# Kernel tuning notes

Measured on AMD Instinct MI355X. Metric: run time of the kernel, lower is better.

The kernel has to match this reference:

```python
import jax, jax.numpy as jnp
import numpy as np

B, S, H, NH = 2, 2048, 2048, 16
HD = H // NH

def setup_inputs() -> dict:
    key = jax.random.key(0)
    ks = jax.random.split(key, 6)
    scale = 1.0 / np.sqrt(H)
    return {
        "x": jax.random.normal(ks[0], (B, S, H), dtype=jnp.float32),
        "Wq": jax.random.normal(ks[1], (H, H), dtype=jnp.float32) * scale,
        "Wk": jax.random.normal(ks[2], (H, H), dtype=jnp.float32) * scale,
        "Wv": jax.random.normal(ks[3], (H, H), dtype=jnp.float32) * scale,
        "Wo": jax.random.normal(ks[4], (H, H), dtype=jnp.float32) * scale,
        "bo": jax.random.normal(ks[5], (H,), dtype=jnp.float32) * 0.01,
    }

def reference(x, Wq, Wk, Wv, Wo, bo):
    # nn.Linear convention: y = x @ W.T (W is [out, in])
    q = (x @ Wq.T).reshape(B, S, NH, HD).transpose(0, 2, 1, 3)  # [B,NH,S,HD]
    k = (x @ Wk.T).reshape(B, S, NH, HD).transpose(0, 2, 1, 3)
    v = (x @ Wv.T).reshape(B, S, NH, HD).transpose(0, 2, 1, 3)
    scale = jnp.asarray(HD, x.dtype) ** -0.5
    scores = jnp.einsum('bhqd,bhkd->bhqk', q, k) * scale  # [B,NH,S,S]
    attn = jax.nn.softmax(scores, axis=-1)
    out = jnp.einsum('bhqk,bhkd->bhqd', attn, v)  # [B,NH,S,HD]
    out = out.transpose(0, 2, 1, 3).reshape(B, S, H)
    return out @ Wo.T + bo
```

## Files before the change

kernel.cpp:

```cpp
#include <hip/hip_runtime.h>
#include <hip/hip_bf16.h>
#include <stdint.h>

#define S_LEN 2048
#define NHEADS 16
#define HDIM 128
#define H_TOT 2048
#define BATCH 2
#define M_TOK 4096
#define KDIM 2048

typedef __attribute__((ext_vector_type(8))) short bf16x8;
typedef __attribute__((ext_vector_type(4))) float f32x4;
typedef __attribute__((ext_vector_type(16))) float f32x16;

__device__ inline ushort bf16rn(float f) {
  union { float f; uint32_t u; } x; x.f = f;
  uint32_t r = x.u + 0x7FFF + ((x.u >> 16) & 1);
  return (ushort)(r >> 16);
}

__global__ __launch_bounds__(256) void cvt_bf16_kernel(const float* __restrict__ in,
                                                       ushort* __restrict__ out, int n4) {
  int i = blockIdx.x * blockDim.x + threadIdx.x;
  int stride = gridDim.x * blockDim.x;
  for (; i < n4; i += stride) {
    float4 v = reinterpret_cast<const float4*>(in)[i];
    ushort4 o;
    o.x = bf16rn(v.x); o.y = bf16rn(v.y); o.z = bf16rn(v.z); o.w = bf16rn(v.w);
    reinterpret_cast<ushort4*>(out)[i] = o;
  }
}

__global__ __launch_bounds__(256) void cvt4_bf16_kernel(const float* __restrict__ w0,
                                                        const float* __restrict__ w1,
                                                        const float* __restrict__ w2,
                                                        const float* __restrict__ w3,
                                                        ushort* __restrict__ o0,
                                                        ushort* __restrict__ o1,
                                                        ushort* __restrict__ o2,
                                                        ushort* __restrict__ o3) {
  const int N4 = KDIM * KDIM / 4;
  int i = blockIdx.x * blockDim.x + threadIdx.x;
  int stride = gridDim.x * blockDim.x;
  for (; i < 4 * N4; i += stride) {
    int seg = i >> 20, off = i & (N4 - 1);
    const float* in = (seg == 0) ? w0 : (seg == 1) ? w1 : (seg == 2) ? w2 : w3;
    ushort* out = (seg == 0) ? o0 : (seg == 1) ? o1 : (seg == 2) ? o2 : o3;
    float4 v = reinterpret_cast<const float4*>(in)[off];
    ushort4 o;
    o.x = bf16rn(v.x); o.y = bf16rn(v.y); o.z = bf16rn(v.z); o.w = bf16rn(v.w);
    reinterpret_cast<ushort4*>(out)[off] = o;
  }
}

template<int MODE>
__global__ __launch_bounds__(256) void gemm_nt(const ushort* __restrict__ A,
                                               const ushort* __restrict__ Bw,
                                               void* __restrict__ Cout,
                                               const float* __restrict__ bias,
                                               float scale) {
  __shared__ ushort As[128 * 32];
  __shared__ ushort Bs[128 * 32];
  const int K = KDIM;
  int tid = threadIdx.x;
  int wave = tid >> 6, lane = tid & 63;
  int bid = blockIdx.x;
  int c = bid & 7, ii = bid >> 3;
  int bx = (c & 1) * 8 + (ii & 7);
  int by = (c >> 1) * 8 + (ii >> 3);
  int bm = by * 128, bn = bx * 128;
  int wr = wave >> 1, wc = wave & 1;

  f32x4 acc[4][4];
#pragma unroll
  for (int i = 0; i < 4; i++)
#pragma unroll
    for (int j = 0; j < 4; j++) acc[i][j] = (f32x4){0.f, 0.f, 0.f, 0.f};

  int r0 = wave * 32 + (lane >> 2);
  int c8 = (lane & 3) * 8;
  const ushort* gA0 = A + (size_t)(bm + r0) * K + c8;
  const ushort* gA1 = gA0 + 16 * (size_t)K;
  const ushort* gB0 = Bw + (size_t)(bn + r0) * K + c8;
  const ushort* gB1 = gB0 + 16 * (size_t)K;
  ushort* lA0 = As + (wave * 2 + 0) * 512;
  ushort* lA1 = As + (wave * 2 + 1) * 512;
  ushort* lB0 = Bs + (wave * 2 + 0) * 512;
  ushort* lB1 = Bs + (wave * 2 + 1) * 512;

  int aoff = (wr * 64 + (lane & 15)) * 32 + (lane >> 4) * 8;
  int boff = (wc * 64 + (lane & 15)) * 32 + (lane >> 4) * 8;

  for (int kt = 0; kt < K; kt += 32) {
    __builtin_amdgcn_global_load_lds((const __attribute__((address_space(1))) void*)gA0,
                                     (__attribute__((address_space(3))) void*)lA0, 16, 0, 0);
    __builtin_amdgcn_global_load_lds((const __attribute__((address_space(1))) void*)gA1,
                                     (__attribute__((address_space(3))) void*)lA1, 16, 0, 0);
    __builtin_amdgcn_global_load_lds((const __attribute__((address_space(1))) void*)gB0,
                                     (__attribute__((address_space(3))) void*)lB0, 16, 0, 0);
    __builtin_amdgcn_global_load_lds((const __attribute__((address_space(1))) void*)gB1,
                                     (__attribute__((address_space(3))) void*)lB1, 16, 0, 0);
    __syncthreads();

    bf16x8 af[4], bfm[4];
#pragma unroll
    for (int i = 0; i < 4; i++) af[i] = *reinterpret_cast<const bf16x8*>(&As[aoff + i * 512]);
#pragma unroll
    for (int j = 0; j < 4; j++) bfm[j] = *reinterpret_cast<const bf16x8*>(&Bs[boff + j * 512]);
#pragma unroll
    for (int i = 0; i < 4; i++)
#pragma unroll
      for (int j = 0; j < 4; j++)
        acc[i][j] = __builtin_amdgcn_mfma_f32_16x16x32_bf16(af[i], bfm[j], acc[i][j], 0, 0, 0);
    __syncthreads();

    gA0 += 32; gA1 += 32; gB0 += 32; gB1 += 32;
  }

  int rbase = bm + wr * 64 + (lane >> 4) * 4;
  int cbase = bn + wc * 64 + (lane & 15);
  if (MODE == 2) {
    float* Cf = (float*)Cout;
#pragma unroll
    for (int j = 0; j < 4; j++) {
      int n = cbase + j * 16;
      float bv = bias[n];
#pragma unroll
      for (int i = 0; i < 4; i++)
#pragma unroll
        for (int q = 0; q < 4; q++) {
          int m = rbase + i * 16 + q;
          Cf[(size_t)m * H_TOT + n] = acc[i][j][q] + bv;
        }
    }
  } else {
    ushort* Cb = (ushort*)Cout;
#pragma unroll
    for (int j = 0; j < 4; j++) {
      int n = cbase + j * 16;
      int h = n >> 7, d = n & 127;
#pragma unroll
      for (int i = 0; i < 4; i++)
#pragma unroll
        for (int q = 0; q < 4; q++) {
          int m = rbase + i * 16 + q;
          int b = m >> 11, s = m & 2047;
          int bh = b * NHEADS + h;
          size_t idx;
          if (MODE == 0) {
            idx = (((size_t)(bh * 64 + (s >> 5)) * 8 + (d >> 4)) * 64 +
                   ((d >> 3) & 1) * 32 + (s & 31)) * 8 + (d & 7);
          } else {
            int r = s & 15;
            int e = (r & 3) | ((r >> 1) & 4);
            int hi = (r >> 2) & 1;
            idx = (((size_t)(bh * 64 + (s >> 5)) * 8 + ((s >> 4) & 1) * 4 + (d >> 5)) * 64 +
                   hi * 32 + (d & 31)) * 8 + e;
          }
          Cb[idx] = bf16rn(acc[i][j][q] * scale);
        }
    }
  }
}

__global__ __launch_bounds__(128) void attn_kernel(const ushort* __restrict__ Qf,
                                                   const ushort* __restrict__ Kf,
                                                   const ushort* __restrict__ Vf,
                                                   ushort* __restrict__ Ob) {
  __shared__ __attribute__((aligned(16))) ushort KV[2][8192];
  __shared__ float lsinv[2][32];
  int lane = threadIdx.x & 63, wave = threadIdx.x >> 6;
  int hi = lane >> 5;

  int bid = blockIdx.x;
  int swz = (bid & 7) * 128 + (bid >> 3);
  int bh = swz >> 5, qt = swz & 31;
  int b = bh >> 4, h = bh & 15;
  int qrow0 = qt * 64 + wave * 32;

  const bf16x8* Qv = reinterpret_cast<const bf16x8*>(Qf) +
                     ((size_t)(bh * 64 + qt * 2 + wave) * 8) * 64 + lane;
  bf16x8 qf[8];
#pragma unroll
  for (int kc = 0; kc < 8; kc++) qf[kc] = Qv[kc * 64];

  f32x16 oacc[4];
#pragma unroll
  for (int d32 = 0; d32 < 4; d32++)
#pragma unroll
    for (int r = 0; r < 16; r++) oacc[d32][r] = 0.f;
  float lsum = 0.f;
  int laneoff = lane * 8;
  const ushort* sbase = wave ? Vf : Kf;

#define STAGE(kt, bufsel)                                                                   \
  {                                                                                         \
    size_t gc = ((size_t)(bh * 64 + (kt))) * 8;                                             \
    _Pragma("unroll") for (int i_ = 0; i_ < 8; i_++) {                                      \
      __builtin_amdgcn_global_load_lds(                                                     \
          (const __attribute__((address_space(1))) void*)(sbase + (gc + i_) * 512 + laneoff),\
          (__attribute__((address_space(3))) void*)(&KV[bufsel][(wave * 8 + i_) * 512]),    \
          16, 0, 0);                                                                        \
    }                                                                                       \
  }

  union pu { bf16x8 v; uint32_t u[4]; };
  pu paA0, paA1, paB0, paB1;
  bf16x8 vrA[8], vrB[8];
  const bf16x8 bz = {0, 0, 0, 0, 0, 0, 0, 0};
#pragma unroll
  for (int j = 0; j < 4; j++) { paA0.u[j] = 0; paA1.u[j] = 0; }
#pragma unroll
  for (int i = 0; i < 8; i++) vrA[i] = bz;

  STAGE(0, 0);
  asm volatile("s_waitcnt vmcnt(0)" ::: "memory");
  __syncthreads();

  const int NT = S_LEN / 32;

#define BODY(T, PI0, PI1, VI, PO0, PO1, VO)                                                 \
  {                                                                                         \
    if ((T) + 1 < NT) STAGE((T) + 1, ((T) + 1) & 1);                                        \
    const ushort* lb = &KV[(T) & 1][0];                                                     \
    f32x16 S;                                                                               \
    _Pragma("unroll") for (int r = 0; r < 16; r++) S[r] = 0.f;                              \
    __builtin_amdgcn_s_setprio(1);                                                          \
    _Pragma("unroll") for (int kc = 0; kc < 8; kc++) {                                      \
      bf16x8 kfr = *reinterpret_cast<const bf16x8*>(&lb[kc * 512 + laneoff]);               \
      S = __builtin_amdgcn_mfma_f32_32x32x16_bf16(kfr, qf[kc], S, 0, 0, 0);                 \
    }                                                                                       \
    _Pragma("unroll") for (int d32 = 0; d32 < 4; d32++) {                                   \
      oacc[d32] = __builtin_amdgcn_mfma_f32_32x32x16_bf16(PI0.v, VI[d32], oacc[d32], 0, 0, 0); \
      oacc[d32] = __builtin_amdgcn_mfma_f32_32x32x16_bf16(PI1.v, VI[4 + d32], oacc[d32], 0, 0, 0); \
    }                                                                                       \
    __builtin_amdgcn_s_setprio(0);                                                          \
    float p_[16];                                                                           \
    _Pragma("unroll") for (int r = 0; r < 16; r++) { p_[r] = exp2f(S[r]); lsum += p_[r]; }  \
    _Pragma("unroll") for (int j = 0; j < 4; j++) {                                         \
      uint32_t w0_, w1_;                                                                    \
      asm("v_cvt_pk_bf16_f32 %0, %1, %2" : "=v"(w0_) : "v"(p_[2 * j]), "v"(p_[2 * j + 1])); \
      asm("v_cvt_pk_bf16_f32 %0, %1, %2" : "=v"(w1_) : "v"(p_[8 + 2 * j]), "v"(p_[9 + 2 * j])); \
      PO0.u[j] = w0_; PO1.u[j] = w1_;                                                       \
    }                                                                                       \
    _Pragma("unroll") for (int i_ = 0; i_ < 8; i_++)                                        \
      VO[i_] = *reinterpret_cast<const bf16x8*>(&lb[4096 + i_ * 512 + laneoff]);            \
    asm volatile("s_waitcnt vmcnt(0)" ::: "memory");                                        \
    __syncthreads();                                                                        \
  }

  for (int t = 0; t < NT; t += 2) {
    BODY(t,     paA0, paA1, vrA, paB0, paB1, vrB);
    BODY(t + 1, paB0, paB1, vrB, paA0, paA1, vrA);
  }
#pragma unroll
  for (int d32 = 0; d32 < 4; d32++) {
    oacc[d32] = __builtin_amdgcn_mfma_f32_32x32x16_bf16(paA0.v, vrA[d32], oacc[d32], 0, 0, 0);
    oacc[d32] = __builtin_amdgcn_mfma_f32_32x32x16_bf16(paA1.v, vrA[4 + d32], oacc[d32], 0, 0, 0);
  }

  float total = lsum + __shfl_xor(lsum, 32);
  if (lane < 32) lsinv[wave][lane] = 1.0f / total;
  __syncthreads();

  float ls[16];
#pragma unroll
  for (int r = 0; r < 16; r++) ls[r] = lsinv[wave][(r & 3) + 8 * (r >> 2) + 4 * hi];
#pragma unroll
  for (int d32 = 0; d32 < 4; d32++)
#pragma unroll
    for (int r = 0; r < 16; r++) {
      int row = (r & 3) + 8 * (r >> 2) + 4 * hi;
      size_t idx = ((size_t)(b * S_LEN + qrow0 + row)) * H_TOT + h * HDIM + d32 * 32 + (lane & 31);
      Ob[idx] = bf16rn(oacc[d32][r] * ls[r]);
    }
#undef BODY
#undef STAGE
}

extern "C" void kernel_launch(void* const* d_in, const int* in_sizes, int n_in,
                              void* d_out, int out_size, void* d_ws, size_t ws_size,
                              hipStream_t stream) {
  const float* x  = (const float*)d_in[0];
  const float* Wq = (const float*)d_in[1];
  const float* Wk = (const float*)d_in[2];
  const float* Wv = (const float*)d_in[3];
  const float* Wo = (const float*)d_in[4];
  const float* bo = (const float*)d_in[5];
  float* out = (float*)d_out;

  char* w = (char*)d_ws;
  ushort* xb  = (ushort*)w; w += (size_t)M_TOK * KDIM * 2;
  ushort* Wqb = (ushort*)w; w += (size_t)KDIM * KDIM * 2;
  ushort* Wkb = (ushort*)w; w += (size_t)KDIM * KDIM * 2;
  ushort* Wvb = (ushort*)w; w += (size_t)KDIM * KDIM * 2;
  ushort* Wob = (ushort*)w; w += (size_t)KDIM * KDIM * 2;
  ushort* Qh  = (ushort*)w; w += (size_t)M_TOK * KDIM * 2;
  ushort* Kh  = (ushort*)w; w += (size_t)M_TOK * KDIM * 2;
  ushort* Vt  = (ushort*)w; w += (size_t)M_TOK * KDIM * 2;
  ushort* Ob  = (ushort*)w; w += (size_t)M_TOK * KDIM * 2;

  hipLaunchKernelGGL(cvt_bf16_kernel, dim3(2048), dim3(256), 0, stream, x, xb, M_TOK * KDIM / 4);
  hipLaunchKernelGGL(cvt4_bf16_kernel, dim3(2048), dim3(256), 0, stream,
                     Wq, Wk, Wv, Wo, Wqb, Wkb, Wvb, Wob);

  const float sl = 0.08838834764831845f * 1.4426950408889634f;
  dim3 g(512), blk(256);
  hipLaunchKernelGGL((gemm_nt<0>), g, blk, 0, stream, xb, Wqb, (void*)Qh, (const float*)nullptr, sl);
  hipLaunchKernelGGL((gemm_nt<0>), g, blk, 0, stream, xb, Wkb, (void*)Kh, (const float*)nullptr, 1.0f);
  hipLaunchKernelGGL((gemm_nt<1>), g, blk, 0, stream, xb, Wvb, (void*)Vt, (const float*)nullptr, 1.0f);

  hipLaunchKernelGGL(attn_kernel, dim3(1024), dim3(128), 0, stream, Qh, Kh, Vt, Ob);

  hipLaunchKernelGGL((gemm_nt<2>), g, blk, 0, stream, Ob, Wob, (void*)out, bo, 1.0f);
}
```

Before: 301.7 us.

## Fuse QKV projections into one pipelined, swizzled 128x256 GEMM kernel

Replaces the single-buffered 128x128 GEMM with a 512-thread 128x256 tile kernel. It uses a K-step of 64, triple-buffered LDS fed by async global-to-LDS loads, an XOR-swizzled LDS layout and waitcnt-based prefetch overlap. The three Q/K/V projections become one launch over a concatenated 6144-wide weight, relying on the contiguous workspace layout, with per-segment output routing and scaling. The aim is to hide global load latency, cut LDS bank conflicts, reduce barrier overhead per FLOP and remove two launches. In exchange it uses about 147KB of LDS per block, which limits occupancy to one block per CU, and it issues redundant prefetches of the first tiles at the end of the loop.

```diff
diff --git a/kernel.cpp b/kernel.cpp
--- a/kernel.cpp
+++ b/kernel.cpp
@@ -54,23 +54,55 @@
   }
 }
 
-template<int MODE>
-__global__ __launch_bounds__(256) void gemm_nt(const ushort* __restrict__ A,
-                                               const ushort* __restrict__ Bw,
-                                               void* __restrict__ Cout,
-                                               const float* __restrict__ bias,
-                                               float scale) {
-  __shared__ ushort As[128 * 32];
-  __shared__ ushort Bs[128 * 32];
+template<int MODE, int NBX>
+__global__ __launch_bounds__(512) void gemm2(const ushort* __restrict__ A,
+                                             const ushort* __restrict__ Bw,
+                                             void* __restrict__ C0,
+                                             void* __restrict__ C1,
+                                             void* __restrict__ C2,
+                                             const float* __restrict__ bias,
+                                             float scale) {
+  __shared__ __attribute__((aligned(16))) char lds[3 * 49152];
   const int K = KDIM;
+  const int NKT = K / 64;
   int tid = threadIdx.x;
   int wave = tid >> 6, lane = tid & 63;
+  int lanelo = lane & 15, lanehi = lane >> 4;
+  int wr = wave >> 2, wc = wave & 3;
+
   int bid = blockIdx.x;
-  int c = bid & 7, ii = bid >> 3;
-  int bx = (c & 1) * 8 + (ii & 7);
-  int by = (c >> 1) * 8 + (ii >> 3);
-  int bm = by * 128, bn = bx * 128;
-  int wr = wave >> 1, wc = wave & 1;
+  const int CHX = NBX / 8;
+  int ii = bid >> 3;
+  int bx = (bid & 7) * CHX + (ii % CHX);
+  int by = ii / CHX;
+  int bm = by * 128, bn = bx * 256;
+
+  const ushort* srcA[2];
+  const ushort* srcB[4];
+#pragma unroll
+  for (int i = 0; i < 2; i++) {
+    int c = i * 512 + tid, row = c >> 3, slot = c & 7;
+    srcA[i] = A + (size_t)(bm + row) * K + ((slot ^ (row & 7)) * 8);
+  }
+#pragma unroll
+  for (int i = 0; i < 4; i++) {
+    int c = i * 512 + tid, row = c >> 3, slot = c & 7;
+    srcB[i] = Bw + (size_t)(bn + row) * K + ((slot ^ (row & 7)) * 8);
+  }
+
+#define STAGE(tile, buf)                                                                    \
+  {                                                                                         \
+    char* dA = lds + (buf) * 49152 + (size_t)tid * 16;                                      \
+    char* dB = lds + (buf) * 49152 + 16384 + (size_t)tid * 16;                              \
+    _Pragma("unroll") for (int i_ = 0; i_ < 2; i_++)                                        \
+      __builtin_amdgcn_global_load_lds(                                                     \
+          (const __attribute__((address_space(1))) void*)(srcA[i_] + (tile) * 64),          \
+          (__attribute__((address_space(3))) void*)(dA + i_ * 8192), 16, 0, 0);             \
+    _Pragma("unroll") for (int i_ = 0; i_ < 4; i_++)                                        \
+      __builtin_amdgcn_global_load_lds(                                                     \
+          (const __attribute__((address_space(1))) void*)(srcB[i_] + (tile) * 64),          \
+          (__attribute__((address_space(3))) void*)(dB + i_ * 8192), 16, 0, 0);             \
+  }
 
   f32x4 acc[4][4];
 #pragma unroll
@@ -78,77 +110,82 @@
 #pragma unroll
     for (int j = 0; j < 4; j++) acc[i][j] = (f32x4){0.f, 0.f, 0.f, 0.f};
 
-  int r0 = wave * 32 + (lane >> 2);
-  int c8 = (lane & 3) * 8;
-  const ushort* gA0 = A + (size_t)(bm + r0) * K + c8;
-  const ushort* gA1 = gA0 + 16 * (size_t)K;
-  const ushort* gB0 = Bw + (size_t)(bn + r0) * K + c8;
-  const ushort* gB1 = gB0 + 16 * (size_t)K;
-  ushort* lA0 = As + (wave * 2 + 0) * 512;
-  ushort* lA1 = As + (wave * 2 + 1) * 512;
-  ushort* lB0 = Bs + (wave * 2 + 0) * 512;
-  ushort* lB1 = Bs + (wave * 2 + 1) * 512;
-
-  int aoff = (wr * 64 + (lane & 15)) * 32 + (lane >> 4) * 8;
-  int boff = (wc * 64 + (lane & 15)) * 32 + (lane >> 4) * 8;
-
-  for (int kt = 0; kt < K; kt += 32) {
-    __builtin_amdgcn_global_load_lds((const __attribute__((address_space(1))) void*)gA0,
-                                     (__attribute__((address_space(3))) void*)lA0, 16, 0, 0);
-    __builtin_amdgcn_global_load_lds((const __attribute__((address_space(1))) void*)gA1,
-                                     (__attribute__((address_space(3))) void*)lA1, 16, 0, 0);
-    __builtin_amdgcn_global_load_lds((const __attribute__((address_space(1))) void*)gB0,
-                                     (__attribute__((address_space(3))) void*)lB0, 16, 0, 0);
-    __builtin_amdgcn_global_load_lds((const __attribute__((address_space(1))) void*)gB1,
-                                     (__attribute__((address_space(3))) void*)lB1, 16, 0, 0);
-    __syncthreads();
-
-    bf16x8 af[4], bfm[4];
-#pragma unroll
-    for (int i = 0; i < 4; i++) af[i] = *reinterpret_cast<const bf16x8*>(&As[aoff + i * 512]);
-#pragma unroll
-    for (int j = 0; j < 4; j++) bfm[j] = *reinterpret_cast<const bf16x8*>(&Bs[boff + j * 512]);
-#pragma unroll
-    for (int i = 0; i < 4; i++)
-#pragma unroll
-      for (int j = 0; j < 4; j++)
-        acc[i][j] = __builtin_amdgcn_mfma_f32_16x16x32_bf16(af[i], bfm[j], acc[i][j], 0, 0, 0);
-    __syncthreads();
-
-    gA0 += 32; gA1 += 32; gB0 += 32; gB1 += 32;
-  }
-
-  int rbase = bm + wr * 64 + (lane >> 4) * 4;
-  int cbase = bn + wc * 64 + (lane & 15);
+  STAGE(0, 0);
+  STAGE(1, 1);
+  asm volatile("s_waitcnt vmcnt(6)" ::: "memory");
+  __builtin_amdgcn_s_barrier();
+  __builtin_amdgcn_sched_barrier(0);
+
+  for (int t = 0; t < NKT; t++) {
+    STAGE((t + 2) & (NKT - 1), (t + 2) % 3);
+
+    const ushort* bufc = (const ushort*)(lds + (t % 3) * 49152);
+
+    bf16x8 bfr[4][2];
+#pragma unroll
+    for (int nf = 0; nf < 4; nf++)
+#pragma unroll
+      for (int kh = 0; kh < 2; kh++) {
+        int row = wc * 64 + nf * 16 + lanelo;
+        int slot = (kh * 4 + lanehi) ^ (row & 7);
+        bfr[nf][kh] = *reinterpret_cast<const bf16x8*>(&bufc[8192 + row * 64 + slot * 8]);
+      }
+
+    __builtin_amdgcn_s_setprio(1);
+#pragma unroll
+    for (int mf = 0; mf < 4; mf++) {
+      int row = wr * 64 + mf * 16 + lanelo;
+      bf16x8 af[2];
+#pragma unroll
+      for (int kh = 0; kh < 2; kh++) {
+        int slot = (kh * 4 + lanehi) ^ (row & 7);
+        af[kh] = *reinterpret_cast<const bf16x8*>(&bufc[row * 64 + slot * 8]);
+      }
+#pragma unroll
+      for (int nf = 0; nf < 4; nf++)
+#pragma unroll
+        for (int kh = 0; kh < 2; kh++)
+          acc[mf][nf] = __builtin_amdgcn_mfma_f32_16x16x32_bf16(af[kh], bfr[nf][kh],
+                                                                acc[mf][nf], 0, 0, 0);
+    }
+    __builtin_amdgcn_s_setprio(0);
+
+    asm volatile("s_waitcnt vmcnt(6)" ::: "memory");
+    __builtin_amdgcn_s_barrier();
+    __builtin_amdgcn_sched_barrier(0);
+  }
+
   if (MODE == 2) {
-    float* Cf = (float*)Cout;
-#pragma unroll
-    for (int j = 0; j < 4; j++) {
-      int n = cbase + j * 16;
+    float* Cf = (float*)C0;
+#pragma unroll
+    for (int nf = 0; nf < 4; nf++) {
+      int n = bn + wc * 64 + nf * 16 + lanelo;
       float bv = bias[n];
 #pragma unroll
-      for (int i = 0; i < 4; i++)
+      for (int mf = 0; mf < 4; mf++)
 #pragma unroll
         for (int q = 0; q < 4; q++) {
-          int m = rbase + i * 16 + q;
-          Cf[(size_t)m * H_TOT + n] = acc[i][j][q] + bv;
+          int m = bm + wr * 64 + mf * 16 + lanehi * 4 + q;
+          Cf[(size_t)m * H_TOT + n] = acc[mf][nf][q] + bv;
         }
     }
   } else {
-    ushort* Cb = (ushort*)Cout;
-#pragma unroll
-    for (int j = 0; j < 4; j++) {
-      int n = cbase + j * 16;
+    int seg = bn >> 11;
+    ushort* dst = (seg == 0) ? (ushort*)C0 : (seg == 1) ? (ushort*)C1 : (ushort*)C2;
+    float sc = (seg == 0) ? scale : 1.0f;
+#pragma unroll
+    for (int nf = 0; nf < 4; nf++) {
+      int n = (bn & 2047) + wc * 64 + nf * 16 + lanelo;
       int h = n >> 7, d = n & 127;
 #pragma unroll
-      for (int i = 0; i < 4; i++)
+      for (int mf = 0; mf < 4; mf++)
 #pragma unroll
         for (int q = 0; q < 4; q++) {
-          int m = rbase + i * 16 + q;
+          int m = bm + wr * 64 + mf * 16 + lanehi * 4 + q;
           int b = m >> 11, s = m & 2047;
           int bh = b * NHEADS + h;
           size_t idx;
-          if (MODE == 0) {
+          if (seg < 2) {
             idx = (((size_t)(bh * 64 + (s >> 5)) * 8 + (d >> 4)) * 64 +
                    ((d >> 3) & 1) * 32 + (s & 31)) * 8 + (d & 7);
           } else {
@@ -158,10 +195,11 @@
             idx = (((size_t)(bh * 64 + (s >> 5)) * 8 + ((s >> 4) & 1) * 4 + (d >> 5)) * 64 +
                    hi * 32 + (d & 31)) * 8 + e;
           }
-          Cb[idx] = bf16rn(acc[i][j][q] * scale);
+          dst[idx] = bf16rn(acc[mf][nf][q] * sc);
         }
     }
   }
+#undef STAGE
 }
 
 __global__ __launch_bounds__(128) void attn_kernel(const ushort* __restrict__ Qf,
@@ -306,12 +344,12 @@
                      Wq, Wk, Wv, Wo, Wqb, Wkb, Wvb, Wob);
 
   const float sl = 0.08838834764831845f * 1.4426950408889634f;
-  dim3 g(512), blk(256);
-  hipLaunchKernelGGL((gemm_nt<0>), g, blk, 0, stream, xb, Wqb, (void*)Qh, (const float*)nullptr, sl);
-  hipLaunchKernelGGL((gemm_nt<0>), g, blk, 0, stream, xb, Wkb, (void*)Kh, (const float*)nullptr, 1.0f);
-  hipLaunchKernelGGL((gemm_nt<1>), g, blk, 0, stream, xb, Wvb, (void*)Vt, (const float*)nullptr, 1.0f);
+
+  hipLaunchKernelGGL((gemm2<0, 24>), dim3(768), dim3(512), 0, stream,
+                     xb, Wqb, (void*)Qh, (void*)Kh, (void*)Vt, (const float*)nullptr, sl);
 
   hipLaunchKernelGGL(attn_kernel, dim3(1024), dim3(128), 0, stream, Qh, Kh, Vt, Ob);
 
-  hipLaunchKernelGGL((gemm_nt<2>), g, blk, 0, stream, Ob, Wob, (void*)out, bo, 1.0f);
-}
+  hipLaunchKernelGGL((gemm2<2, 8>), dim3(256), dim3(512), 0, stream,
+                     Ob, Wob, (void*)out, nullptr, nullptr, bo, 1.0f);
+}
```

New measurement: 271.0 us. 10.2% less time.
